# Performance work log

Measured on AMD Instinct MI355X. Metric: run time of the kernel, lower is better.

Reference implementation:

```python
import jax, jax.numpy as jnp
import numpy as np

NUM_HEADS = 8
GROUPS = 32
EPS = 1e-5


def group_norm(x, gamma, beta):
    # x: [b, c, l]; normalize over (c//GROUPS, l) per group
    b, c, l = x.shape
    xg = x.reshape(b, GROUPS, -1)
    mu = jnp.mean(xg, axis=-1, keepdims=True)
    var = jnp.mean(jnp.square(xg - mu), axis=-1, keepdims=True)
    xn = ((xg - mu) * jax.lax.rsqrt(var + EPS)).reshape(b, c, l)
    return xn * gamma[None, :, None] + beta[None, :, None]


def setup_inputs() -> dict:
    key = jax.random.key(0)
    ks = jax.random.split(key, 8)
    b, c, h, w = 8, 512, 64, 64
    cc, cl = 768, 256
    inner = 512
    s = lambda fan_in: 1.0 / np.sqrt(fan_in)
    return {
        "x": jax.random.normal(ks[0], (b, c, h, w), jnp.float32),
        "context": jax.random.normal(ks[1], (b, cc, cl), jnp.float32),
        "gnx_g": jnp.ones((c,), jnp.float32),
        "gnx_b": jnp.zeros((c,), jnp.float32),
        "gnc_g": jnp.ones((cc,), jnp.float32),
        "gnc_b": jnp.zeros((cc,), jnp.float32),
        "wq": jax.random.normal(ks[2], (inner, c), jnp.float32) * s(c),
        "bq": jax.random.normal(ks[3], (inner,), jnp.float32) * s(c),
        "wkv": jax.random.normal(ks[4], (2 * inner, cc), jnp.float32) * s(cc),
        "bkv": jax.random.normal(ks[5], (2 * inner,), jnp.float32) * s(cc),
        "wo": jax.random.normal(ks[6], (c, inner), jnp.float32) * s(inner),
        "bo": jax.random.normal(ks[7], (c,), jnp.float32) * s(inner),
    }


def reference(x, context, gnx_g, gnx_b, gnc_g, gnc_b, wq, bq, wkv, bkv, wo, bo):
    b, c, h, w = x.shape
    xf = x.reshape(b, c, h * w)                      # [b, c, L]
    inner = wq.shape[0]
    dh = inner // NUM_HEADS
    scale = dh ** (-0.5)

    q = jnp.einsum('oc,bcl->bol', wq, group_norm(xf, gnx_g, gnx_b)) + bq[None, :, None]
    kv = jnp.einsum('oc,bcl->bol', wkv, group_norm(context, gnc_g, gnc_b)) + bkv[None, :, None]
    k, v = jnp.split(kv, 2, axis=1)                  # [b, inner, S] each

    L = xf.shape[-1]
    S = k.shape[-1]
    q = q.reshape(b * NUM_HEADS, dh, L)
    k = k.reshape(b * NUM_HEADS, dh, S)
    v = v.reshape(b * NUM_HEADS, dh, S)

    # Faithful double-scale quirk: effective scaling is 1/dh
    dots = jnp.einsum('bct,bcs->bts', q * scale, k * scale)   # [bH, L, S]
    attn = jax.nn.softmax(dots.astype(jnp.float32), axis=-1).astype(dots.dtype)
    out = jnp.einsum('bts,bcs->bct', attn, v)                 # [bH, dh, L]
    out = out.reshape(b, inner, L)
    out = jnp.einsum('oc,bcl->bol', wo, out) + bo[None, :, None]
    return (xf + out).reshape(b, c, h, w)
```

## Files before the change

### kernel.cpp

```cpp
#include <hip/hip_runtime.h>

typedef unsigned short u16;
typedef unsigned int u32;
typedef __bf16 bf16x8 __attribute__((ext_vector_type(8)));
typedef float f32x4 __attribute__((ext_vector_type(4)));

__device__ __forceinline__ u16 f2bf(float f) {
    return __builtin_bit_cast(u16, (__bf16)f);
}
__device__ __forceinline__ u32 pkbf(float a, float b) {
    return (u32)__builtin_bit_cast(u16, (__bf16)a) |
           ((u32)__builtin_bit_cast(u16, (__bf16)b) << 16);
}
__device__ __forceinline__ u32 pku(u16 a, u16 b) {
    return (u32)a | ((u32)b << 16);
}
__device__ __forceinline__ bf16x8 ldb8(const void* p) {
    return __builtin_bit_cast(bf16x8, *(const uint4*)p);
}
__device__ __forceinline__ f32x4 mfma16(bf16x8 a, bf16x8 b, f32x4 c) {
    return __builtin_amdgcn_mfma_f32_16x16x32_bf16(a, b, c, 0, 0, 0);
}

__global__ __launch_bounds__(256) void cvt_w(const float* __restrict__ in,
                                             u16* __restrict__ out, int n4) {
    int i = blockIdx.x * 256 + threadIdx.x;
    const int stride = gridDim.x * 256;
    for (; i < n4; i += stride) {
        float4 v = ((const float4*)in)[i];
        ((uint2*)out)[i] = make_uint2(pkbf(v.x, v.y), pkbf(v.z, v.w));
    }
}

__global__ __launch_bounds__(256) void gn_stats(const float* __restrict__ in,
                                                float2* __restrict__ stats, int N) {
    const int tid = threadIdx.x;
    const long base = (long)blockIdx.x * N;
    float s = 0.f, s2 = 0.f;
    for (int i = tid * 4; i < N; i += 256 * 4) {
        float4 v = *(const float4*)(in + base + i);
        s += v.x + v.y + v.z + v.w;
        s2 += v.x * v.x + v.y * v.y + v.z * v.z + v.w * v.w;
    }
#pragma unroll
    for (int m = 1; m < 64; m <<= 1) { s += __shfl_xor(s, m); s2 += __shfl_xor(s2, m); }
    __shared__ float ps[4], ps2[4];
    const int w = tid >> 6;
    if ((tid & 63) == 0) { ps[w] = s; ps2[w] = s2; }
    __syncthreads();
    if (tid == 0) {
        float S = ps[0] + ps[1] + ps[2] + ps[3];
        float S2 = ps2[0] + ps2[1] + ps2[2] + ps2[3];
        float mu = S / (float)N;
        float var = S2 / (float)N - mu * mu;
        stats[blockIdx.x] = make_float2(mu, rsqrtf(var + 1e-5f));
    }
}


__global__ __launch_bounds__(256) void gn_tr(const float* __restrict__ ctx,
                                             const float2* __restrict__ stats,
                                             const float* __restrict__ gamma,
                                             const float* __restrict__ beta,
                                             u16* __restrict__ ctx_t) {
    __shared__ u16 T[64][64];
    const int tid = threadIdx.x;
    const int b = blockIdx.z;
    const int c0 = blockIdx.x * 64, s0 = blockIdx.y * 64;
#pragma unroll
    for (int r = 0; r < 4; ++r) {
        int idx = r * 256 + tid;
        int c = idx >> 4, s4 = (idx & 15) << 2;
        int cg = c0 + c;
        float4 v = *(const float4*)(ctx + ((long)b * 768 + cg) * 256 + s0 + s4);
        float2 st = stats[b * 32 + cg / 24];
        float gm = gamma[cg], bt = beta[cg];
        float vv[4] = {(v.x - st.x) * st.y * gm + bt, (v.y - st.x) * st.y * gm + bt,
                       (v.z - st.x) * st.y * gm + bt, (v.w - st.x) * st.y * gm + bt};
#pragma unroll
        for (int jj = 0; jj < 4; ++jj) {
            int j = (jj + (tid & 3)) & 3;
            int row = s4 + j;
            T[row][c ^ ((row & 7) << 3)] = f2bf(vv[j]);
        }
    }
    __syncthreads();
#pragma unroll
    for (int r = 0; r < 2; ++r) {
        int f = r * 256 + tid;
        int s = f >> 3, cf = (f & 7) << 3;
        uint4 vv = *(const uint4*)&T[s][cf ^ ((s & 7) << 3)];
        *(uint4*)(ctx_t + ((long)b * 256 + s0 + s) * 768 + c0 + cf) = vv;
    }
}

__global__ __launch_bounds__(256, 2) void gemm_kv2(
    const u16* __restrict__ W, const u16* __restrict__ ctx_t,
    const float* __restrict__ bias, u16* __restrict__ k_t, u16* __restrict__ vout) {
    constexpr int K = 768;
    const int tid = threadIdx.x;
    const int b = blockIdx.z;
    const int o0 = blockIdx.x * 64;
    const int s0 = blockIdx.y * 64;
    const int lane = tid & 63, wv = tid >> 6;
    const int l16 = lane & 15, g = lane >> 4;

    const u16* ap = W + (long)(o0 + wv * 16 + l16) * K;
    const u16* ct = ctx_t + ((long)b * 256 + s0) * K;

    f32x4 acc[4] = {};
#pragma unroll
    for (int kc = 0; kc < 24; ++kc) {
        const int k8 = kc * 32 + g * 8;
        bf16x8 afr = ldb8(ap + k8);
#pragma unroll
        for (int ni = 0; ni < 4; ++ni) {
            bf16x8 bfr = ldb8(ct + (long)(ni * 16 + l16) * K + k8);
            acc[ni] = mfma16(afr, bfr, acc[ni]);
        }
    }
    const int orow = o0 + wv * 16 + g * 4;
    if (blockIdx.x < 8) {
        const int h = blockIdx.x;
        const int d0 = wv * 16 + g * 4;
        const float b0 = bias[orow], b1 = bias[orow + 1];
        const float b2 = bias[orow + 2], b3 = bias[orow + 3];
#pragma unroll
        for (int ni = 0; ni < 4; ++ni) {
            int s = s0 + ni * 16 + l16;
            *(uint2*)(k_t + (((long)b * 8 + h) * 256 + s) * 64 + d0) =
                make_uint2(pkbf(acc[ni][0] + b0, acc[ni][1] + b1),
                           pkbf(acc[ni][2] + b2, acc[ni][3] + b3));
        }
    } else {
#pragma unroll
        for (int ni = 0; ni < 4; ++ni) {
            int s = s0 + ni * 16 + l16;
#pragma unroll
            for (int i = 0; i < 4; ++i) {
                int vr = orow - 512 + i;
                vout[((long)b * 512 + vr) * 256 + s] = f2bf(acc[ni][i] + bias[orow + i]);
            }
        }
    }
}

template <int MODE>
__global__ __launch_bounds__(256, 2) void big_gemm(
    const u16* __restrict__ W, const void* __restrict__ Bsrc,
    const float2* __restrict__ stats, const float* __restrict__ gamma,
    const float* __restrict__ beta, const float* __restrict__ bias,
    const float* __restrict__ X, void* __restrict__ outp) {
    constexpr int K = 512, N = 4096, CPG = 16;
    __shared__ u16 Blds[64][64];
    const int tid = threadIdx.x;
    const int b = blockIdx.z;
    const int n0 = blockIdx.x * 64;
    const int lane = tid & 63, w = tid >> 6;
    const int l16 = lane & 15, g = lane >> 4;

    f32x4 acc[8][4] = {};
    for (int c = 0; c < 8; ++c) {
        const int k0 = c * 64;
        __syncthreads();
        if (MODE == 0) {
            const float* Bb = (const float*)Bsrc + (long)b * K * N;
#pragma unroll
            for (int r = 0; r < 4; ++r) {
                int idx = r * 256 + tid;
                int kk = idx >> 4;
                int n4 = (idx & 15) << 2;
                int kg = k0 + kk;
                float4 v = *(const float4*)(Bb + (long)kg * N + n0 + n4);
                float2 st = stats[b * 32 + kg / CPG];
                float gm = gamma[kg], bt = beta[kg];
                v.x = (v.x - st.x) * st.y * gm + bt;
                v.y = (v.y - st.x) * st.y * gm + bt;
                v.z = (v.z - st.x) * st.y * gm + bt;
                v.w = (v.w - st.x) * st.y * gm + bt;
                float vv[4] = {v.x, v.y, v.z, v.w};
#pragma unroll
                for (int jj = 0; jj < 4; ++jj) {
                    int j = (jj + (lane & 3)) & 3;
                    int row = n4 + j;
                    Blds[row][kk ^ ((row & 7) << 3)] = f2bf(vv[j]);
                }
            }
        } else {
            const u16* Ob = (const u16*)Bsrc + (((long)b * 8 + c) * 4096 + n0) * 64;
#pragma unroll
            for (int r = 0; r < 2; ++r) {
                int idx = r * 256 + tid;
                int t = idx >> 3;
                int d0 = (idx & 7) << 3;
                uint4 vv = *(const uint4*)(Ob + (long)t * 64 + d0);
                *(uint4*)&Blds[t][d0 ^ ((t & 7) << 3)] = vv;
            }
        }
        __syncthreads();
#pragma unroll
        for (int kk = 0; kk < 2; ++kk) {
            bf16x8 bfr[4];
#pragma unroll
            for (int ni = 0; ni < 4; ++ni) {
                int row = ni * 16 + l16;
                bfr[ni] = ldb8(&Blds[row][(kk * 32 + g * 8) ^ ((row & 7) << 3)]);
            }
#pragma unroll
            for (int mi = 0; mi < 8; ++mi) {
                int arow = w * 128 + mi * 16 + l16;
                bf16x8 afr = ldb8(W + (long)arow * K + k0 + kk * 32 + g * 8);
#pragma unroll
                for (int ni = 0; ni < 4; ++ni)
                    acc[mi][ni] = mfma16(afr, bfr[ni], acc[mi][ni]);
            }
        }
    }
    if (MODE == 0) {
        u16* qt = (u16*)outp;
#pragma unroll
        for (int mi = 0; mi < 8; ++mi) {
            int h = w * 2 + (mi >> 2);
            int dbase = (mi & 3) * 16 + g * 4;
#pragma unroll
            for (int ni = 0; ni < 4; ++ni) {
                int col = n0 + ni * 16 + l16;
                float v0 = acc[mi][ni][0] + bias[h * 64 + dbase + 0];
                float v1 = acc[mi][ni][1] + bias[h * 64 + dbase + 1];
                float v2 = acc[mi][ni][2] + bias[h * 64 + dbase + 2];
                float v3 = acc[mi][ni][3] + bias[h * 64 + dbase + 3];
                *(uint2*)(qt + (((long)b * 8 + h) * 4096 + col) * 64 + dbase) =
                    make_uint2(pkbf(v0, v1), pkbf(v2, v3));
            }
        }
    } else {
        float* out = (float*)outp;
        const long ob = (long)b * K * N;
#pragma unroll
        for (int mi = 0; mi < 8; ++mi)
#pragma unroll
            for (int i = 0; i < 4; ++i) {
                int row = w * 128 + mi * 16 + g * 4 + i;
                float bs = bias[row];
#pragma unroll
                for (int ni = 0; ni < 4; ++ni) {
                    int col = n0 + ni * 16 + l16;
                    long off = ob + (long)row * N + col;
                    out[off] = acc[mi][ni][i] + bs + X[off];
                }
            }
    }
}

__global__ __launch_bounds__(256, 1) void attn_v7(const u16* __restrict__ qt_in,
                                                  const u16* __restrict__ k_t,
                                                  const u16* __restrict__ v,
                                                  u16* __restrict__ qt_out) {
    __shared__ u16 kT[256][64];
    __shared__ u16 Vp[64][256];
    const int tid = threadIdx.x;
    const int bh = blockIdx.y;
    const int b = bh >> 3, h = bh & 7;
    const int lane = tid & 63, w = tid >> 6;
    const int l16 = lane & 15, g = lane >> 4;

    const long kb = (long)bh * 256 * 64;
    const long vb = ((long)(b * 512 + h * 64)) * 256;
    const long qb = (long)bh * 4096 * 64 + (long)blockIdx.x * 512 * 64;

#pragma unroll
    for (int r = 0; r < 8; ++r) {
        int idx = r * 256 + tid;
        int s = idx >> 3, d0 = (idx & 7) << 3;
        uint4 vv = *(const uint4*)(k_t + kb + (long)s * 64 + d0);
        *(uint4*)&kT[s][d0 ^ ((s & 7) << 3)] = vv;
    }
#pragma unroll
    for (int r = 0; r < 8; ++r) {
        int idx = r * 256 + tid;
        int d = idx >> 5, s0 = (idx & 31) << 3;
        union { uint4 v4; u16 h8[8]; } u;
        u.v4 = *(const uint4*)(v + vb + (long)d * 256 + s0);
        int f = s0 >> 4, g2 = (s0 >> 2) & 3;
        int cl = ((f >> 1) << 5) + (g2 << 3) + ((f & 1) << 2);
        int sw = (d & 7) << 3;
        *(uint2*)&Vp[d][cl ^ sw] = make_uint2(pku(u.h8[0], u.h8[1]), pku(u.h8[2], u.h8[3]));
        *(uint2*)&Vp[d][(cl + 8) ^ sw] = make_uint2(pku(u.h8[4], u.h8[5]), pku(u.h8[6], u.h8[7]));
    }
    __syncthreads();

    const float aa = 0.015625f * 1.44269504f;
    for (int it = 0; it < 8; ++it) {
        const int tcol = it * 64 + w * 16 + l16;
        const u16* qp = qt_in + qb + (long)tcol * 64;
        bf16x8 bq0 = ldb8(qp + g * 8);
        bf16x8 bq1 = ldb8(qp + 32 + g * 8);
        f32x4 sacc[16] = {};
#pragma unroll
        for (int mc = 0; mc < 4; ++mc) {
#pragma unroll
            for (int kk = 0; kk < 2; ++kk) {
                bf16x8 bqk = kk ? bq1 : bq0;
#pragma unroll
                for (int j = 0; j < 4; ++j) {
                    int mi = mc * 4 + j;
                    bf16x8 ak = ldb8(&kT[mi * 16 + l16][(kk * 32 + g * 8) ^ ((l16 & 7) << 3)]);
                    sacc[mi] = mfma16(ak, bqk, sacc[mi]);
                }
            }
        }
        float m = -3e38f;
#pragma unroll
        for (int f = 0; f < 16; ++f)
#pragma unroll
            for (int i = 0; i < 4; ++i) m = fmaxf(m, sacc[f][i]);
        m = fmaxf(m, __shfl_xor(m, 16));
        m = fmaxf(m, __shfl_xor(m, 32));
        float m2 = m * aa;
        float sum = 0.f;
#pragma unroll
        for (int f = 0; f < 16; ++f)
#pragma unroll
            for (int i = 0; i < 4; ++i) {
                float p = exp2f(fmaf(sacc[f][i], aa, -m2));
                sacc[f][i] = p;
                sum += p;
            }
        sum += __shfl_xor(sum, 16);
        sum += __shfl_xor(sum, 32);
        const float inv = 1.0f / sum;
        f32x4 oacc[4] = {};
#pragma unroll
        for (int ks = 0; ks < 8; ++ks) {
            bf16x8 bp = __builtin_bit_cast(bf16x8,
                make_uint4(pkbf(sacc[2 * ks][0], sacc[2 * ks][1]),
                           pkbf(sacc[2 * ks][2], sacc[2 * ks][3]),
                           pkbf(sacc[2 * ks + 1][0], sacc[2 * ks + 1][1]),
                           pkbf(sacc[2 * ks + 1][2], sacc[2 * ks + 1][3])));
#pragma unroll
            for (int mi = 0; mi < 4; ++mi) {
                bf16x8 av = ldb8(&Vp[mi * 16 + l16][(ks * 32 + g * 8) ^ ((l16 & 7) << 3)]);
                oacc[mi] = mfma16(av, bp, oacc[mi]);
            }
        }
        u16* op = qt_out + qb + (long)tcol * 64;
#pragma unroll
        for (int mi = 0; mi < 4; ++mi) {
            *(uint2*)(op + mi * 16 + g * 4) = make_uint2(
                pkbf(oacc[mi][0] * inv, oacc[mi][1] * inv),
                pkbf(oacc[mi][2] * inv, oacc[mi][3] * inv));
        }
    }
}

template <bool GN, bool RESID>
__global__ __launch_bounds__(256, 2) void big_gemm_f32(
    const u16* __restrict__ W, const float* __restrict__ B,
    const float2* __restrict__ stats, const float* __restrict__ gamma,
    const float* __restrict__ beta, const float* __restrict__ bias,
    const float* __restrict__ X, float* __restrict__ out) {
    constexpr int K = 512, N = 4096, CPG = 16;
    __shared__ u16 Blds[64][64];
    const int tid = threadIdx.x;
    const int b = blockIdx.z;
    const int n0 = blockIdx.x * 64;
    const int lane = tid & 63, w = tid >> 6;
    const int l16 = lane & 15, g = lane >> 4;
    const float* Bb = B + (long)b * K * N;

    f32x4 acc[8][4] = {};
    for (int c = 0; c < 8; ++c) {
        const int k0 = c * 64;
        __syncthreads();
#pragma unroll
        for (int r = 0; r < 4; ++r) {
            int idx = r * 256 + tid;
            int kk = idx >> 4;
            int n4 = (idx & 15) << 2;
            int kg = k0 + kk;
            float4 v = *(const float4*)(Bb + (long)kg * N + n0 + n4);
            if (GN) {
                float2 st = stats[b * 32 + kg / CPG];
                float gm = gamma[kg], bt = beta[kg];
                v.x = (v.x - st.x) * st.y * gm + bt;
                v.y = (v.y - st.x) * st.y * gm + bt;
                v.z = (v.z - st.x) * st.y * gm + bt;
                v.w = (v.w - st.x) * st.y * gm + bt;
            }
            float vv[4] = {v.x, v.y, v.z, v.w};
#pragma unroll
            for (int jj = 0; jj < 4; ++jj) {
                int j = (jj + (lane & 3)) & 3;
                int row = n4 + j;
                Blds[row][kk ^ ((row & 7) << 3)] = f2bf(vv[j]);
            }
        }
        __syncthreads();
#pragma unroll
        for (int kk = 0; kk < 2; ++kk) {
            bf16x8 bfr[4];
#pragma unroll
            for (int ni = 0; ni < 4; ++ni) {
                int row = ni * 16 + l16;
                bfr[ni] = ldb8(&Blds[row][(kk * 32 + g * 8) ^ ((row & 7) << 3)]);
            }
#pragma unroll
            for (int mi = 0; mi < 8; ++mi) {
                int arow = w * 128 + mi * 16 + l16;
                bf16x8 afr = ldb8(W + (long)arow * K + k0 + kk * 32 + g * 8);
#pragma unroll
                for (int ni = 0; ni < 4; ++ni)
                    acc[mi][ni] = mfma16(afr, bfr[ni], acc[mi][ni]);
            }
        }
    }
    const long ob = (long)b * K * N;
#pragma unroll
    for (int mi = 0; mi < 8; ++mi)
#pragma unroll
        for (int i = 0; i < 4; ++i) {
            int row = w * 128 + mi * 16 + g * 4 + i;
            float bs = bias[row];
#pragma unroll
            for (int ni = 0; ni < 4; ++ni) {
                int col = n0 + ni * 16 + l16;
                long off = ob + (long)row * N + col;
                float v = acc[mi][ni][i] + bs;
                if (RESID) v += X[off];
                out[off] = v;
            }
        }
}

__global__ __launch_bounds__(256) void gemm_kv_old(
    const u16* __restrict__ W, const float* __restrict__ act,
    const float2* __restrict__ stats, const float* __restrict__ gamma,
    const float* __restrict__ beta, const float* __restrict__ bias,
    u16* __restrict__ outp, int K, int N, int CPG, long actBS, long outBS) {
    __shared__ u16 Blds[128][40];
    const int tid = threadIdx.x;
    const int b = blockIdx.z;
    const int m0 = blockIdx.y * 128;
    const int n0 = blockIdx.x * 128;
    const int lane = tid & 63;
    const int w = tid >> 6;
    const int wr = w >> 1, wc = w & 1;
    const int l16 = lane & 15, g = lane >> 4;

    const float* actB = act + (long)b * actBS;
    f32x4 acc[4][4] = {};
    for (int s = 0; s < K / 32; ++s) {
        const int k0 = s * 32;
        __syncthreads();
#pragma unroll
        for (int r = 0; r < 4; ++r) {
            int idx = r * 256 + tid;
            int kk = idx >> 5;
            int n4 = (idx & 31) << 2;
            int kg = k0 + kk;
            float2 st = stats[b * 32 + kg / CPG];
            float gm = gamma[kg], bt = beta[kg];
            float4 v = *(const float4*)(actB + (long)kg * N + n0 + n4);
            Blds[n4 + 0][kk] = f2bf((v.x - st.x) * st.y * gm + bt);
            Blds[n4 + 1][kk] = f2bf((v.y - st.x) * st.y * gm + bt);
            Blds[n4 + 2][kk] = f2bf((v.z - st.x) * st.y * gm + bt);
            Blds[n4 + 3][kk] = f2bf((v.w - st.x) * st.y * gm + bt);
        }
        __syncthreads();
        bf16x8 bfr[4];
#pragma unroll
        for (int ni = 0; ni < 4; ++ni)
            bfr[ni] = ldb8(&Blds[wc * 64 + ni * 16 + l16][g * 8]);
#pragma unroll
        for (int mi = 0; mi < 4; ++mi) {
            int row = m0 + wr * 64 + mi * 16 + l16;
            bf16x8 afr = ldb8(W + (long)row * K + k0 + g * 8);
#pragma unroll
            for (int ni = 0; ni < 4; ++ni)
                acc[mi][ni] = mfma16(afr, bfr[ni], acc[mi][ni]);
        }
    }
#pragma unroll
    for (int mi = 0; mi < 4; ++mi)
#pragma unroll
        for (int i = 0; i < 4; ++i) {
            int row = m0 + wr * 64 + mi * 16 + g * 4 + i;
            float bs = bias[row];
#pragma unroll
            for (int ni = 0; ni < 4; ++ni) {
                int col = n0 + wc * 64 + ni * 16 + l16;
                outp[(long)b * outBS + (long)row * N + col] = f2bf(acc[mi][ni][i] + bs);
            }
        }
}

__global__ __launch_bounds__(256, 2) void attn_v4(const float* q,
                                                  const u16* __restrict__ kv,
                                                  float* out) {
    __shared__ u16 kT[256][64];
    __shared__ u16 Vp[64][256];
    const int tid = threadIdx.x;
    const int bh = blockIdx.y;
    const int b = bh >> 3, h = bh & 7;
    const int lane = tid & 63, w = tid >> 6;
    const int l16 = lane & 15, g = lane >> 4;

    const long kbase = ((long)(b * 1024 + h * 64)) * 256;
    const long vbase = ((long)(b * 1024 + 512 + h * 64)) * 256;
    const long qb = ((long)(b * 512 + h * 64)) * 4096 + blockIdx.x * 512;

#pragma unroll
    for (int r = 0; r < 8; ++r) {
        int idx = r * 256 + tid;
        int d = idx >> 5, s8 = idx & 31;
        union { uint4 v; u16 h8[8]; } u;
        u.v = *(const uint4*)(kv + kbase + (long)d * 256 + s8 * 8);
#pragma unroll
        for (int j = 0; j < 8; ++j)
            kT[s8 * 8 + j][d ^ (j << 3)] = u.h8[j];
    }
#pragma unroll
    for (int r = 0; r < 8; ++r) {
        int idx = r * 256 + tid;
        int d = idx >> 5, s0 = (idx & 31) << 3;
        union { uint4 v; u16 h8[8]; } u;
        u.v = *(const uint4*)(kv + vbase + (long)d * 256 + s0);
        int f = s0 >> 4, g2 = (s0 >> 2) & 3;
        int cl = ((f >> 1) << 5) + (g2 << 3) + ((f & 1) << 2);
        int sw = (d & 7) << 3;
        *(uint2*)&Vp[d][cl ^ sw] = make_uint2(pku(u.h8[0], u.h8[1]), pku(u.h8[2], u.h8[3]));
        *(uint2*)&Vp[d][(cl + 8) ^ sw] = make_uint2(pku(u.h8[4], u.h8[5]), pku(u.h8[6], u.h8[7]));
    }
    __syncthreads();

    const float aa = 0.015625f * 1.44269504f;
    for (int it = 0; it < 8; ++it) {
        const int tcol = it * 64 + w * 16 + l16;
        u32 bqw[2][4];
#pragma unroll
        for (int kk = 0; kk < 2; ++kk) {
            const float* qp = q + qb + tcol + (long)(kk * 32 + g * 8) * 4096;
#pragma unroll
            for (int jp = 0; jp < 4; ++jp)
                bqw[kk][jp] = pkbf(qp[(2 * jp) * 4096], qp[(2 * jp + 1) * 4096]);
        }
        f32x4 sacc[16] = {};
#pragma unroll
        for (int kk = 0; kk < 2; ++kk) {
            bf16x8 bq_ = __builtin_bit_cast(bf16x8,
                make_uint4(bqw[kk][0], bqw[kk][1], bqw[kk][2], bqw[kk][3]));
#pragma unroll
            for (int mi = 0; mi < 16; ++mi) {
                bf16x8 ak = ldb8(&kT[mi * 16 + l16][(kk * 32 + g * 8) ^ ((l16 & 7) << 3)]);
                sacc[mi] = mfma16(ak, bq_, sacc[mi]);
            }
        }
        float m = -3e38f;
#pragma unroll
        for (int f = 0; f < 16; ++f)
#pragma unroll
            for (int i = 0; i < 4; ++i) m = fmaxf(m, sacc[f][i]);
        m = fmaxf(m, __shfl_xor(m, 16));
        m = fmaxf(m, __shfl_xor(m, 32));
        float m2 = m * aa;
        float sum = 0.f;
#pragma unroll
        for (int f = 0; f < 16; ++f)
#pragma unroll
            for (int i = 0; i < 4; ++i) {
                float p = exp2f(fmaf(sacc[f][i], aa, -m2));
                sacc[f][i] = p;
                sum += p;
            }
        sum += __shfl_xor(sum, 16);
        sum += __shfl_xor(sum, 32);
        const float inv = 1.0f / sum;
        f32x4 oacc[4] = {};
#pragma unroll
        for (int ks = 0; ks < 8; ++ks) {
            bf16x8 bp = __builtin_bit_cast(bf16x8,
                make_uint4(pkbf(sacc[2 * ks][0], sacc[2 * ks][1]),
                           pkbf(sacc[2 * ks][2], sacc[2 * ks][3]),
                           pkbf(sacc[2 * ks + 1][0], sacc[2 * ks + 1][1]),
                           pkbf(sacc[2 * ks + 1][2], sacc[2 * ks + 1][3])));
#pragma unroll
            for (int mi = 0; mi < 4; ++mi) {
                bf16x8 av = ldb8(&Vp[mi * 16 + l16][(ks * 32 + g * 8) ^ ((l16 & 7) << 3)]);
                oacc[mi] = mfma16(av, bp, oacc[mi]);
            }
        }
#pragma unroll
        for (int mi = 0; mi < 4; ++mi)
#pragma unroll
            for (int i = 0; i < 4; ++i)
                out[qb + (long)(mi * 16 + g * 4 + i) * 4096 + tcol] = oacc[mi][i] * inv;
    }
}

extern "C" void kernel_launch(void* const* d_in, const int* in_sizes, int n_in,
                              void* d_out, int out_size, void* d_ws, size_t ws_size,
                              hipStream_t stream) {
    const float* x     = (const float*)d_in[0];
    const float* ctx   = (const float*)d_in[1];
    const float* gnx_g = (const float*)d_in[2];
    const float* gnx_b = (const float*)d_in[3];
    const float* gnc_g = (const float*)d_in[4];
    const float* gnc_b = (const float*)d_in[5];
    const float* wq    = (const float*)d_in[6];
    const float* bq    = (const float*)d_in[7];
    const float* wkv   = (const float*)d_in[8];
    const float* bkv   = (const float*)d_in[9];
    const float* wo    = (const float*)d_in[10];
    const float* bo    = (const float*)d_in[11];
    float* out = (float*)d_out;

    char* ws = (char*)d_ws;
    float2* stats_x = (float2*)ws;
    float2* stats_c = (float2*)(ws + 2048);
    u16* wq_bf  = (u16*)(ws + 4096);
    u16* wkv_bf = (u16*)(ws + 528384);
    u16* wo_bf  = (u16*)(ws + 2101248);

    cvt_w<<<dim3(256), dim3(256), 0, stream>>>(wq, wq_bf, 512 * 512 / 4);
    cvt_w<<<dim3(256), dim3(256), 0, stream>>>(wkv, wkv_bf, 1024 * 768 / 4);
    cvt_w<<<dim3(256), dim3(256), 0, stream>>>(wo, wo_bf, 512 * 512 / 4);
    gn_stats<<<dim3(256), dim3(256), 0, stream>>>(x, stats_x, 16 * 4096);
    gn_stats<<<dim3(256), dim3(256), 0, stream>>>(ctx, stats_c, 24 * 256);

    const size_t NEED = 40374272;
    if (ws_size >= NEED) {
        u16* k_t   = (u16*)(ws + 2625536);
        u16* v     = (u16*)(ws + 4722688);
        u16* q_t   = (u16*)(ws + 6819840);
        u16* ctx_t = (u16*)(ws + 6819840);

        gn_tr<<<dim3(12, 4, 8), dim3(256), 0, stream>>>(
            ctx, stats_c, gnc_g, gnc_b, ctx_t);
        gemm_kv2<<<dim3(16, 4, 8), dim3(256), 0, stream>>>(
            wkv_bf, ctx_t, bkv, k_t, v);
        big_gemm<0><<<dim3(64, 1, 8), dim3(256), 0, stream>>>(
            wq_bf, x, stats_x, gnx_g, gnx_b, bq, nullptr, q_t);
        attn_v7<<<dim3(8, 64), dim3(256), 0, stream>>>(q_t, k_t, v, q_t);
        big_gemm<1><<<dim3(64, 1, 8), dim3(256), 0, stream>>>(
            wo_bf, q_t, nullptr, nullptr, nullptr, bo, x, out);
    } else {
        u16* kv = (u16*)(ws + 2625536);
        big_gemm_f32<true, false><<<dim3(64, 1, 8), dim3(256), 0, stream>>>(
            wq_bf, x, stats_x, gnx_g, gnx_b, bq, nullptr, out);
        gemm_kv_old<<<dim3(2, 8, 8), dim3(256), 0, stream>>>(
            wkv_bf, ctx, stats_c, gnc_g, gnc_b, bkv, kv, 768, 256, 24,
            (long)768 * 256, (long)1024 * 256);
        attn_v4<<<dim3(8, 64), dim3(256), 0, stream>>>(out, kv, out);
        big_gemm_f32<false, true><<<dim3(64, 1, 8), dim3(256), 0, stream>>>(
            wo_bf, out, nullptr, nullptr, nullptr, bo, x, out);
    }
}
```

Before: 230.8 us.

## Double-buffer out-projection GEMM via direct global-to-LDS loads, merge weight conversions

The out-projection path of big_gemm now uses double-buffered LDS tiles filled with global_load_lds, so the next K-chunk is prefetched while MFMAs run on the current one, with a single barrier per iteration. The swizzle moves to the global source address because the direct LDS write lands at a fixed lane-linear location. The three weight-conversion launches are merged into one 2D-grid kernel, and gn_stats uses 1024-thread blocks for more parallelism per group. The cost is extra LDS for the second buffer, which may affect occupancy, and reliance on correct synchronisation of the asynchronous LDS loads.

```diff
diff --git a/kernel.cpp b/kernel.cpp
--- a/kernel.cpp
+++ b/kernel.cpp
@@ -21,9 +21,21 @@
 __device__ __forceinline__ f32x4 mfma16(bf16x8 a, bf16x8 b, f32x4 c) {
     return __builtin_amdgcn_mfma_f32_16x16x32_bf16(a, b, c, 0, 0, 0);
 }
-
-__global__ __launch_bounds__(256) void cvt_w(const float* __restrict__ in,
-                                             u16* __restrict__ out, int n4) {
+__device__ __forceinline__ void gload_lds16(const void* g, void* l) {
+    __builtin_amdgcn_global_load_lds(
+        (const __attribute__((address_space(1))) unsigned int*)g,
+        (__attribute__((address_space(3))) unsigned int*)l, 16, 0, 0);
+}
+
+__global__ __launch_bounds__(256) void cvt_w3(const float* __restrict__ w0,
+                                              const float* __restrict__ w1,
+                                              const float* __restrict__ w2,
+                                              u16* __restrict__ o0, u16* __restrict__ o1,
+                                              u16* __restrict__ o2) {
+    const int which = blockIdx.y;
+    const float* in = which == 0 ? w0 : which == 1 ? w1 : w2;
+    u16* out = which == 0 ? o0 : which == 1 ? o1 : o2;
+    const int n4 = which == 1 ? 196608 : 65536;
     int i = blockIdx.x * 256 + threadIdx.x;
     const int stride = gridDim.x * 256;
     for (; i < n4; i += stride) {
@@ -32,25 +44,26 @@
     }
 }
 
-__global__ __launch_bounds__(256) void gn_stats(const float* __restrict__ in,
-                                                float2* __restrict__ stats, int N) {
+__global__ __launch_bounds__(1024) void gn_stats(const float* __restrict__ in,
+                                                 float2* __restrict__ stats, int N) {
     const int tid = threadIdx.x;
     const long base = (long)blockIdx.x * N;
     float s = 0.f, s2 = 0.f;
-    for (int i = tid * 4; i < N; i += 256 * 4) {
+    for (int i = tid * 4; i < N; i += 1024 * 4) {
         float4 v = *(const float4*)(in + base + i);
         s += v.x + v.y + v.z + v.w;
         s2 += v.x * v.x + v.y * v.y + v.z * v.z + v.w * v.w;
     }
 #pragma unroll
     for (int m = 1; m < 64; m <<= 1) { s += __shfl_xor(s, m); s2 += __shfl_xor(s2, m); }
-    __shared__ float ps[4], ps2[4];
+    __shared__ float ps[16], ps2[16];
     const int w = tid >> 6;
     if ((tid & 63) == 0) { ps[w] = s; ps2[w] = s2; }
     __syncthreads();
     if (tid == 0) {
-        float S = ps[0] + ps[1] + ps[2] + ps[3];
-        float S2 = ps2[0] + ps2[1] + ps2[2] + ps2[3];
+        float S = 0.f, S2 = 0.f;
+#pragma unroll
+        for (int k = 0; k < 16; ++k) { S += ps[k]; S2 += ps2[k]; }
         float mu = S / (float)N;
         float var = S2 / (float)N - mu * mu;
         stats[blockIdx.x] = make_float2(mu, rsqrtf(var + 1e-5f));
@@ -152,7 +165,7 @@
     const float* __restrict__ beta, const float* __restrict__ bias,
     const float* __restrict__ X, void* __restrict__ outp) {
     constexpr int K = 512, N = 4096, CPG = 16;
-    __shared__ u16 Blds[64][64];
+    __shared__ u16 Blds[2][64][64];
     const int tid = threadIdx.x;
     const int b = blockIdx.z;
     const int n0 = blockIdx.x * 64;
@@ -160,10 +173,52 @@
     const int l16 = lane & 15, g = lane >> 4;
 
     f32x4 acc[8][4] = {};
-    for (int c = 0; c < 8; ++c) {
-        const int k0 = c * 64;
+
+    if (MODE == 1) {
+        const u16* Ob0 = (const u16*)Bsrc + ((long)b * 8) * 4096 * 64 + (long)n0 * 64;
+#pragma unroll
+        for (int r = 0; r < 2; ++r) {
+            int idx = r * 256 + tid;
+            int t = idx >> 3, d0 = (idx & 7) << 3;
+            gload_lds16(Ob0 + (long)t * 64 + (d0 ^ ((t & 7) << 3)), &Blds[0][t][d0]);
+        }
         __syncthreads();
-        if (MODE == 0) {
+        for (int c = 0; c < 8; ++c) {
+            const int cur = c & 1;
+            if (c < 7) {
+                const u16* Obn = Ob0 + (long)(c + 1) * 4096 * 64;
+#pragma unroll
+                for (int r = 0; r < 2; ++r) {
+                    int idx = r * 256 + tid;
+                    int t = idx >> 3, d0 = (idx & 7) << 3;
+                    gload_lds16(Obn + (long)t * 64 + (d0 ^ ((t & 7) << 3)),
+                                &Blds[cur ^ 1][t][d0]);
+                }
+            }
+            const int k0 = c * 64;
+#pragma unroll
+            for (int kk = 0; kk < 2; ++kk) {
+                bf16x8 bfr[4];
+#pragma unroll
+                for (int ni = 0; ni < 4; ++ni) {
+                    int row = ni * 16 + l16;
+                    bfr[ni] = ldb8(&Blds[cur][row][(kk * 32 + g * 8) ^ ((row & 7) << 3)]);
+                }
+#pragma unroll
+                for (int mi = 0; mi < 8; ++mi) {
+                    int arow = w * 128 + mi * 16 + l16;
+                    bf16x8 afr = ldb8(W + (long)arow * K + k0 + kk * 32 + g * 8);
+#pragma unroll
+                    for (int ni = 0; ni < 4; ++ni)
+                        acc[mi][ni] = mfma16(afr, bfr[ni], acc[mi][ni]);
+                }
+            }
+            __syncthreads();
+        }
+    } else {
+        for (int c = 0; c < 8; ++c) {
+            const int k0 = c * 64;
+            __syncthreads();
             const float* Bb = (const float*)Bsrc + (long)b * K * N;
 #pragma unroll
             for (int r = 0; r < 4; ++r) {
@@ -183,39 +238,30 @@
                 for (int jj = 0; jj < 4; ++jj) {
                     int j = (jj + (lane & 3)) & 3;
                     int row = n4 + j;
-                    Blds[row][kk ^ ((row & 7) << 3)] = f2bf(vv[j]);
+                    Blds[0][row][kk ^ ((row & 7) << 3)] = f2bf(vv[j]);
                 }
             }
-        } else {
-            const u16* Ob = (const u16*)Bsrc + (((long)b * 8 + c) * 4096 + n0) * 64;
-#pragma unroll
-            for (int r = 0; r < 2; ++r) {
-                int idx = r * 256 + tid;
-                int t = idx >> 3;
-                int d0 = (idx & 7) << 3;
-                uint4 vv = *(const uint4*)(Ob + (long)t * 64 + d0);
-                *(uint4*)&Blds[t][d0 ^ ((t & 7) << 3)] = vv;
-            }
-        }
-        __syncthreads();
-#pragma unroll
-        for (int kk = 0; kk < 2; ++kk) {
-            bf16x8 bfr[4];
-#pragma unroll
-            for (int ni = 0; ni < 4; ++ni) {
-                int row = ni * 16 + l16;
-                bfr[ni] = ldb8(&Blds[row][(kk * 32 + g * 8) ^ ((row & 7) << 3)]);
-            }
-#pragma unroll
-            for (int mi = 0; mi < 8; ++mi) {
-                int arow = w * 128 + mi * 16 + l16;
-                bf16x8 afr = ldb8(W + (long)arow * K + k0 + kk * 32 + g * 8);
-#pragma unroll
-                for (int ni = 0; ni < 4; ++ni)
-                    acc[mi][ni] = mfma16(afr, bfr[ni], acc[mi][ni]);
-            }
-        }
-    }
+            __syncthreads();
+#pragma unroll
+            for (int kk = 0; kk < 2; ++kk) {
+                bf16x8 bfr[4];
+#pragma unroll
+                for (int ni = 0; ni < 4; ++ni) {
+                    int row = ni * 16 + l16;
+                    bfr[ni] = ldb8(&Blds[0][row][(kk * 32 + g * 8) ^ ((row & 7) << 3)]);
+                }
+#pragma unroll
+                for (int mi = 0; mi < 8; ++mi) {
+                    int arow = w * 128 + mi * 16 + l16;
+                    bf16x8 afr = ldb8(W + (long)arow * K + k0 + kk * 32 + g * 8);
+#pragma unroll
+                    for (int ni = 0; ni < 4; ++ni)
+                        acc[mi][ni] = mfma16(afr, bfr[ni], acc[mi][ni]);
+                }
+            }
+        }
+    }
+
     if (MODE == 0) {
         u16* qt = (u16*)outp;
 #pragma unroll
@@ -621,11 +667,9 @@
     u16* wkv_bf = (u16*)(ws + 528384);
     u16* wo_bf  = (u16*)(ws + 2101248);
 
-    cvt_w<<<dim3(256), dim3(256), 0, stream>>>(wq, wq_bf, 512 * 512 / 4);
-    cvt_w<<<dim3(256), dim3(256), 0, stream>>>(wkv, wkv_bf, 1024 * 768 / 4);
-    cvt_w<<<dim3(256), dim3(256), 0, stream>>>(wo, wo_bf, 512 * 512 / 4);
-    gn_stats<<<dim3(256), dim3(256), 0, stream>>>(x, stats_x, 16 * 4096);
-    gn_stats<<<dim3(256), dim3(256), 0, stream>>>(ctx, stats_c, 24 * 256);
+    cvt_w3<<<dim3(128, 3), dim3(256), 0, stream>>>(wq, wkv, wo, wq_bf, wkv_bf, wo_bf);
+    gn_stats<<<dim3(256), dim3(1024), 0, stream>>>(x, stats_x, 16 * 4096);
+    gn_stats<<<dim3(256), dim3(1024), 0, stream>>>(ctx, stats_c, 24 * 256);
 
     const size_t NEED = 40374272;
     if (ws_size >= NEED) {
```

Measured after the change: 213.0 us. 7.7% less time.
